# Performance work log

Hardware: AMD Instinct MI355X
Metric: run time of the kernel (lower is better)

Reference implementation:

```python
import jax, jax.numpy as jnp
import numpy as np

H_DIM = 1024
N_HEADS = 16
HEAD_D = H_DIM // N_HEADS  # 64


def setup_inputs() -> dict:
    key = jax.random.key(0)
    ks = jax.random.split(key, 10)
    B, T, C = 2, 2048, H_DIM
    init = 1.0 / np.sqrt(C)  # lecun_normal-scale stand-in
    src = jax.random.normal(ks[0], (B, T, C), dtype=jnp.float32)
    mask = jnp.ones((B, T), dtype=jnp.float32)  # unused when causal
    Wq = jax.random.normal(ks[1], (C, H_DIM), dtype=jnp.float32) * init
    Wk = jax.random.normal(ks[2], (C, H_DIM), dtype=jnp.float32) * init
    Wv = jax.random.normal(ks[3], (C, H_DIM), dtype=jnp.float32) * init
    Wo = jax.random.normal(ks[4], (H_DIM, H_DIM), dtype=jnp.float32) * init
    bq = jnp.zeros((H_DIM,), jnp.float32)
    bk = jnp.zeros((H_DIM,), jnp.float32)
    bv = jnp.zeros((H_DIM,), jnp.float32)
    bo = jnp.zeros((H_DIM,), jnp.float32)
    return {"src": src, "mask": mask, "Wq": Wq, "bq": bq, "Wk": Wk, "bk": bk,
            "Wv": Wv, "bv": bv, "Wo": Wo, "bo": bo}


def reference(src, mask, Wq, bq, Wk, bk, Wv, bv, Wo, bo):
    # MaskedCausalAttention forward, deterministic=True (dropout = identity),
    # use_causal_mask=True.
    B, T, C = src.shape
    N, D = N_HEADS, HEAD_D
    # q,k,v: [B, N, T, D]
    q = (src @ Wq + bq).reshape(B, T, N, D).transpose(0, 2, 1, 3)
    k = (src @ Wk + bk).reshape(B, T, N, D).transpose(0, 2, 1, 3)
    v = (src @ Wv + bv).reshape(B, T, N, D).transpose(0, 2, 1, 3)
    # scores: [B, N, T, T]
    scores = jnp.einsum('bntd,bnsd->bnts', q, k) / jnp.sqrt(jnp.float32(D))
    causal = jnp.tril(jnp.ones((T, T), dtype=bool))[None, None]
    scores = jnp.where(causal, scores, -jnp.inf)
    probs = jax.nn.softmax(scores, axis=-1)
    attn = jnp.einsum('bnts,bnsd->bntd', probs, v)  # [B, N, T, D]
    attn = attn.transpose(0, 2, 1, 3).reshape(B, T, N * D)
    return attn @ Wo + bo
```

## Files before the change

kernel.cpp:

```cpp
#include <hip/hip_runtime.h>
#include <hip/hip_bf16.h>

typedef __hip_bfloat16 bf16;
typedef __attribute__((ext_vector_type(8))) short short8;
typedef __attribute__((ext_vector_type(4))) float f32x4;

#define BATCH 2
#define SEQ   2048
#define HDIM  1024
#define NHEAD 16
#define DHEAD 64
#define MROWS (BATCH*SEQ)

#define QSCALE 0.18033688f
#define EXP2F(x) __builtin_amdgcn_exp2f(x)

static __device__ __forceinline__ short f2bs(float x) {
    __hip_bfloat16 h = (__hip_bfloat16)x;
    return *reinterpret_cast<short*>(&h);
}
static __device__ __forceinline__ unsigned int pk2(float a, float b) {
    __hip_bfloat162 h = __float22bfloat162_rn(make_float2(a, b));
    return *reinterpret_cast<unsigned int*>(&h);
}

static __device__ __forceinline__ void gload16(const void* g, void* l) {
    __builtin_amdgcn_global_load_lds(
        (const __attribute__((address_space(1))) unsigned int*)g,
        (__attribute__((address_space(3))) unsigned int*)l, 16, 0, 0);
}

__global__ __launch_bounds__(256) void prep1(const float* __restrict__ src,
        const float* __restrict__ Wq, const float* __restrict__ Wk,
        const float* __restrict__ Wv,
        short* __restrict__ Sb, short* __restrict__ WqkT,
        short* __restrict__ WvT)
{
    __shared__ float t[64][65];
    const int bx = blockIdx.x, tid = threadIdx.x;
    if (bx < 4096) {
        int i = bx * 256 + tid;
        float4 v = ((const float4*)src)[i];
        ushort4 o;
        o.x = (unsigned short)f2bs(v.x);
        o.y = (unsigned short)f2bs(v.y);
        o.z = (unsigned short)f2bs(v.z);
        o.w = (unsigned short)f2bs(v.w);
        ((ushort4*)Sb)[i] = o;
        return;
    }
    const int tb = bx - 4096;
    const int wsel = tb >> 8;
    const float* W = (wsel == 0) ? Wq : (wsel == 1) ? Wk : Wv;
    short* dst = (wsel < 2) ? WqkT : WvT;
    const int roff = (wsel < 2) ? wsel * 1024 : 0;
    const int t8 = tb & 255;
    const int n0 = (t8 & 15) * 64, k0 = (t8 >> 4) * 64;
#pragma unroll
    for (int i = 0; i < 16; i++) {
        int idx = tid + i * 256, r = idx >> 6, c = idx & 63;
        t[r][c] = W[(size_t)(k0 + r) * HDIM + n0 + c];
    }
    __syncthreads();
#pragma unroll
    for (int i = 0; i < 16; i++) {
        int idx = tid + i * 256, c = idx >> 6, r = idx & 63;
        dst[(size_t)(roff + n0 + c) * HDIM + k0 + r] = f2bs(t[r][c]);
    }
}

__global__ __launch_bounds__(256) void gemm_qk(const short* __restrict__ A,
        const short* __restrict__ Bt,
        const float* __restrict__ bq, const float* __restrict__ bk,
        short* __restrict__ Qout, short* __restrict__ Kout)
{
    __shared__ short As[2][8 * 512];
    __shared__ short Bs[2][8 * 512];
    const int tid = threadIdx.x, lane = tid & 63, w = tid >> 6;
    const int quad = lane >> 4, l15 = lane & 15;
    const int m0 = blockIdx.y * 128, n0 = blockIdx.x * 128;
    const int wr = w >> 1, wc = w & 1;

    const short* gsrc[4];
    short* dst0[4];
    short* dst1[4];
#pragma unroll
    for (int i = 0; i < 4; i++) {
        int u = w * 4 + i;
        if (u < 8) {
            gsrc[i] = A + (size_t)(m0 + u * 16 + l15) * HDIM + quad * 8;
            dst0[i] = &As[0][u * 512];
            dst1[i] = &As[1][u * 512];
        } else {
            int c = u - 8;
            gsrc[i] = Bt + (size_t)(n0 + c * 16 + l15) * HDIM + quad * 8;
            dst0[i] = &Bs[0][c * 512];
            dst1[i] = &Bs[1][c * 512];
        }
    }

    f32x4 acc[4][4];
#pragma unroll
    for (int i = 0; i < 4; i++)
#pragma unroll
        for (int j = 0; j < 4; j++) acc[i][j] = (f32x4){0.f, 0.f, 0.f, 0.f};

#pragma unroll
    for (int i = 0; i < 4; i++) { gload16(gsrc[i], dst0[i]); gsrc[i] += 32; }
    __syncthreads();

    for (int kk = 0; kk < 32; ++kk) {
        const int cur = kk & 1;
        if (kk < 31) {
#pragma unroll
            for (int i = 0; i < 4; i++) {
                gload16(gsrc[i], cur ? dst0[i] : dst1[i]);
                gsrc[i] += 32;
            }
        }
        short8 af[4], bfr[4];
#pragma unroll
        for (int mi = 0; mi < 4; mi++)
            af[mi] = *(const short8*)&As[cur][(wr * 4 + mi) * 512 + lane * 8];
#pragma unroll
        for (int ni = 0; ni < 4; ni++)
            bfr[ni] = *(const short8*)&Bs[cur][(wc * 4 + ni) * 512 + lane * 8];
#pragma unroll
        for (int mi = 0; mi < 4; mi++)
#pragma unroll
            for (int ni = 0; ni < 4; ni++)
                acc[mi][ni] = __builtin_amdgcn_mfma_f32_16x16x32_bf16(
                                  af[mi], bfr[ni], acc[mi][ni], 0, 0, 0);
        __syncthreads();
    }

    const int region = n0 >> 10;
    const float* bias = region ? bk : bq;
    const float oscale = region ? 1.0f : QSCALE;
    short* C = region ? Kout : Qout;

#pragma unroll
    for (int mi = 0; mi < 4; mi++) {
        int mB = m0 + (wr * 4 + mi) * 16 + quad * 4;
#pragma unroll
        for (int ni = 0; ni < 4; ni++) {
            int nl = (n0 + (wc * 4 + ni) * 16 + l15) & 1023;
            float bb = bias[nl];
#pragma unroll
            for (int r = 0; r < 4; r++)
                C[(size_t)(mB + r) * HDIM + nl] =
                    f2bs((acc[mi][ni][r] + bb) * oscale);
        }
    }
}

__global__ __launch_bounds__(256) void gemm_v(const short* __restrict__ A,
        const short* __restrict__ Bt, const float* __restrict__ bv,
        short* __restrict__ Vtout)
{
    __shared__ short As[2][4 * 512];
    __shared__ short Bs[2][8 * 512];
    const int tid = threadIdx.x, lane = tid & 63, w = tid >> 6;
    const int quad = lane >> 4, l15 = lane & 15;
    const int m0 = blockIdx.y * 64, n0 = blockIdx.x * 128;
    const int wr = w >> 1, wc = w & 1;

    const short* gsrc[3];
    short* dst0[3];
    short* dst1[3];
#pragma unroll
    for (int i = 0; i < 3; i++) {
        int u = w * 3 + i;
        if (u < 4) {
            gsrc[i] = A + (size_t)(m0 + u * 16 + l15) * HDIM + quad * 8;
            dst0[i] = &As[0][u * 512];
            dst1[i] = &As[1][u * 512];
        } else {
            int c = u - 4;
            gsrc[i] = Bt + (size_t)(n0 + c * 16 + l15) * HDIM + quad * 8;
            dst0[i] = &Bs[0][c * 512];
            dst1[i] = &Bs[1][c * 512];
        }
    }

    f32x4 acc[2][4];
#pragma unroll
    for (int i = 0; i < 2; i++)
#pragma unroll
        for (int j = 0; j < 4; j++) acc[i][j] = (f32x4){0.f, 0.f, 0.f, 0.f};

#pragma unroll
    for (int i = 0; i < 3; i++) { gload16(gsrc[i], dst0[i]); gsrc[i] += 32; }
    __syncthreads();

    for (int kk = 0; kk < 32; ++kk) {
        const int cur = kk & 1;
        if (kk < 31) {
#pragma unroll
            for (int i = 0; i < 3; i++) {
                gload16(gsrc[i], cur ? dst0[i] : dst1[i]);
                gsrc[i] += 32;
            }
        }
        short8 af[2], bfr[4];
#pragma unroll
        for (int mi = 0; mi < 2; mi++)
            af[mi] = *(const short8*)&As[cur][(wr * 2 + mi) * 512 + lane * 8];
#pragma unroll
        for (int ni = 0; ni < 4; ni++)
            bfr[ni] = *(const short8*)&Bs[cur][(wc * 4 + ni) * 512 + lane * 8];
#pragma unroll
        for (int mi = 0; mi < 2; mi++)
#pragma unroll
            for (int ni = 0; ni < 4; ni++)
                acc[mi][ni] = __builtin_amdgcn_mfma_f32_16x16x32_bf16(
                                  af[mi], bfr[ni], acc[mi][ni], 0, 0, 0);
        __syncthreads();
    }

#pragma unroll
    for (int mi = 0; mi < 2; mi++) {
        int mB = m0 + (wr * 2 + mi) * 16 + quad * 4;
        int bb = mB >> 11, t = mB & 2047;
#pragma unroll
        for (int ni = 0; ni < 4; ni++) {
            int n = n0 + (wc * 4 + ni) * 16 + l15;
            int h = n >> 6, d = n & 63;
            float bvv = bv[n];
            size_t base = ((size_t)((bb * NHEAD + h) * DHEAD + d)) * SEQ + t;
            ushort4 pk;
            pk.x = (unsigned short)f2bs(acc[mi][ni][0] + bvv);
            pk.y = (unsigned short)f2bs(acc[mi][ni][1] + bvv);
            pk.z = (unsigned short)f2bs(acc[mi][ni][2] + bvv);
            pk.w = (unsigned short)f2bs(acc[mi][ni][3] + bvv);
            *(ushort4*)(Vtout + base) = pk;
        }
    }
}

__global__ __launch_bounds__(256) void gemm_o(const short* __restrict__ A,
        const short* __restrict__ Bt, const float* __restrict__ bo,
        float* __restrict__ Out)
{
    __shared__ short As[2][4 * 512];
    __shared__ short Bs[2][8 * 512];
    const int tid = threadIdx.x, lane = tid & 63, w = tid >> 6;
    const int quad = lane >> 4, l15 = lane & 15;
    const int m0 = blockIdx.y * 64, n0 = blockIdx.x * 128;
    const int wr = w >> 1, wc = w & 1;

    const short* gsrc[3];
    short* dst0[3];
    short* dst1[3];
#pragma unroll
    for (int i = 0; i < 3; i++) {
        int u = w * 3 + i;
        if (u < 4) {
            gsrc[i] = A + (size_t)(m0 + u * 16 + l15) * HDIM + quad * 8;
            dst0[i] = &As[0][u * 512];
            dst1[i] = &As[1][u * 512];
        } else {
            int c = u - 4;
            gsrc[i] = Bt + (size_t)(n0 + c * 16 + l15) * HDIM + quad * 8;
            dst0[i] = &Bs[0][c * 512];
            dst1[i] = &Bs[1][c * 512];
        }
    }

    f32x4 acc[2][4];
#pragma unroll
    for (int i = 0; i < 2; i++)
#pragma unroll
        for (int j = 0; j < 4; j++) acc[i][j] = (f32x4){0.f, 0.f, 0.f, 0.f};

#pragma unroll
    for (int i = 0; i < 3; i++) { gload16(gsrc[i], dst0[i]); gsrc[i] += 32; }
    __syncthreads();

    for (int kk = 0; kk < 32; ++kk) {
        const int cur = kk & 1;
        if (kk < 31) {
#pragma unroll
            for (int i = 0; i < 3; i++) {
                gload16(gsrc[i], cur ? dst0[i] : dst1[i]);
                gsrc[i] += 32;
            }
        }
        short8 af[2], bfr[4];
#pragma unroll
        for (int mi = 0; mi < 2; mi++)
            af[mi] = *(const short8*)&As[cur][(wr * 2 + mi) * 512 + lane * 8];
#pragma unroll
        for (int ni = 0; ni < 4; ni++)
            bfr[ni] = *(const short8*)&Bs[cur][(wc * 4 + ni) * 512 + lane * 8];
#pragma unroll
        for (int mi = 0; mi < 2; mi++)
#pragma unroll
            for (int ni = 0; ni < 4; ni++)
                acc[mi][ni] = __builtin_amdgcn_mfma_f32_16x16x32_bf16(
                                  af[mi], bfr[ni], acc[mi][ni], 0, 0, 0);
        __syncthreads();
    }

#pragma unroll
    for (int mi = 0; mi < 2; mi++) {
        int mB = m0 + (wr * 2 + mi) * 16 + quad * 4;
#pragma unroll
        for (int ni = 0; ni < 4; ni++) {
            int n = n0 + (wc * 4 + ni) * 16 + l15;
            float bb = bo[n];
#pragma unroll
            for (int r = 0; r < 4; r++)
                Out[(size_t)(mB + r) * HDIM + n] = acc[mi][ni][r] + bb;
        }
    }
}

__global__ __launch_bounds__(256) void attn_mfma(const short* __restrict__ Qb,
        const short* __restrict__ Kb, const short* __restrict__ Vt,
        short* __restrict__ Ab,
        const float* __restrict__ Wo, short* __restrict__ WoT)
{
    __shared__ short SMEM[21248];
    short* Ks = SMEM;
    short* Vs = SMEM + 8192;
    short* Ps = SMEM + 16384;
    const int tid = threadIdx.x, lane = tid & 63, w = tid >> 6;
    const int quad = lane >> 4, l15 = lane & 15;

    if (blockIdx.x == 16) {
        float* t = (float*)SMEM;
        const int bsel = blockIdx.z * 16 + blockIdx.y;
#pragma unroll
        for (int j = 0; j < 8; j++) {
            int t8 = bsel * 8 + j;
            int n0 = (t8 & 15) * 64, k0 = (t8 >> 4) * 64;
            __syncthreads();
#pragma unroll
            for (int i = 0; i < 16; i++) {
                int idx = tid + i * 256, r = idx >> 6, c = idx & 63;
                t[r * 65 + c] = Wo[(size_t)(k0 + r) * HDIM + n0 + c];
            }
            __syncthreads();
#pragma unroll
            for (int i = 0; i < 16; i++) {
                int idx = tid + i * 256, c = idx >> 6, r = idx & 63;
                WoT[(size_t)(n0 + c) * HDIM + k0 + r] = f2bs(t[r * 65 + c]);
            }
        }
        return;
    }

    const int L = blockIdx.x + 16 * (blockIdx.y + 16 * blockIdx.z);
    const int slot = L >> 3;
    const int pair = (L & 7) * 4 + (slot >> 4);
    const int strip0 = slot & 15;
    const int b = pair >> 4, head = pair & 15;

    const short* Kbh = Kb + (size_t)b * SEQ * HDIM + head * DHEAD;
    const short* Vth = Vt + (size_t)(b * NHEAD + head) * DHEAD * SEQ;
    short* Pw = &Ps[w * 1152];

    auto stage = [&](int s0, int bf) {
#pragma unroll
        for (int i = 0; i < 4; i++) {
            int u = w * 4 + i;
            if (u < 8) {
                int t = u >> 1, h = u & 1;
                const short* g = Kbh + (size_t)(s0 + t * 16 + l15) * HDIM
                                 + h * 32 + quad * 8;
                gload16(g, &Ks[bf * 4096 + u * 512]);
            } else {
                int c = u - 8, dt = c >> 1, kh = c & 1;
                const short* g = Vth + (size_t)(dt * 16 + l15) * SEQ
                                 + s0 + kh * 32 + quad * 8;
                gload16(g, &Vs[bf * 4096 + c * 512]);
            }
        }
    };

    const int strips[2] = { strip0, 31 - strip0 };

    for (int si = 0; si < 2; ++si) {
        const int strip = strips[si];
        const int qbase = strip * 64;
        const int qr = qbase + w * 16 + l15;

        const short* qptr = Qb + (size_t)(b * SEQ + qr) * HDIM + head * DHEAD + quad * 8;
        short8 bq0 = *(const short8*)qptr;
        short8 bq1 = *(const short8*)(qptr + 32);

        f32x4 o[4];
#pragma unroll
        for (int dt = 0; dt < 4; dt++) o[dt] = (f32x4){0.f, 0.f, 0.f, 0.f};
        float psum = 0.f;

        stage(0, 0);
        __syncthreads();

        for (int it = 0; it <= strip; ++it) {
            const int s0 = it * 64;
            const int cur = it & 1;
            if (it < strip) stage(s0 + 64, cur ^ 1);

            f32x4 sv[4];
#pragma unroll
            for (int t = 0; t < 4; t++) {
                sv[t] = (f32x4){0.f, 0.f, 0.f, 0.f};
                short8 k0 = *(const short8*)&Ks[cur * 4096 + (t * 2) * 512 + lane * 8];
                short8 k1 = *(const short8*)&Ks[cur * 4096 + (t * 2 + 1) * 512 + lane * 8];
                sv[t] = __builtin_amdgcn_mfma_f32_16x16x32_bf16(k0, bq0, sv[t], 0, 0, 0);
                sv[t] = __builtin_amdgcn_mfma_f32_16x16x32_bf16(k1, bq1, sv[t], 0, 0, 0);
            }

            float p[16];
            if (it == strip) {
#pragma unroll
                for (int t = 0; t < 4; t++)
#pragma unroll
                    for (int r = 0; r < 4; r++) {
                        int key = s0 + t * 16 + quad * 4 + r;
                        p[t * 4 + r] = (key <= qr) ? EXP2F(sv[t][r]) : 0.f;
                    }
            } else {
#pragma unroll
                for (int t = 0; t < 4; t++)
#pragma unroll
                    for (int r = 0; r < 4; r++)
                        p[t * 4 + r] = EXP2F(sv[t][r]);
            }
#pragma unroll
            for (int i = 0; i < 16; i++) psum += p[i];

#pragma unroll
            for (int t = 0; t < 4; t++) {
                uint2 u2;
                u2.x = pk2(p[t * 4],     p[t * 4 + 1]);
                u2.y = pk2(p[t * 4 + 2], p[t * 4 + 3]);
                *(uint2*)&Pw[l15 * 72 + t * 16 + quad * 4] = u2;
            }
            short8 bp0 = *(const short8*)&Pw[l15 * 72 + quad * 8];
            short8 bp1 = *(const short8*)&Pw[l15 * 72 + 32 + quad * 8];

#pragma unroll
            for (int dt = 0; dt < 4; dt++) {
                short8 av0 = *(const short8*)&Vs[cur * 4096 + (dt * 2) * 512 + lane * 8];
                short8 av1 = *(const short8*)&Vs[cur * 4096 + (dt * 2 + 1) * 512 + lane * 8];
                o[dt] = __builtin_amdgcn_mfma_f32_16x16x32_bf16(av0, bp0, o[dt], 0, 0, 0);
                o[dt] = __builtin_amdgcn_mfma_f32_16x16x32_bf16(av1, bp1, o[dt], 0, 0, 0);
            }
            __syncthreads();
        }

        float lrow = psum + __shfl_xor(psum, 16);
        lrow += __shfl_xor(lrow, 32);
        const float inv = 1.f / lrow;

        const size_t obase = (size_t)(b * SEQ + qr) * HDIM + head * DHEAD;
#pragma unroll
        for (int dt = 0; dt < 4; dt++) {
            uint2 u2;
            u2.x = pk2(o[dt][0] * inv, o[dt][1] * inv);
            u2.y = pk2(o[dt][2] * inv, o[dt][3] * inv);
            *(uint2*)&Ab[obase + dt * 16 + quad * 4] = u2;
        }
    }
}

extern "C" void kernel_launch(void* const* d_in, const int* in_sizes, int n_in,
                              void* d_out, int out_size, void* d_ws, size_t ws_size,
                              hipStream_t stream)
{
    const float* src = (const float*)d_in[0];
    const float* Wq = (const float*)d_in[2];
    const float* bq = (const float*)d_in[3];
    const float* Wk = (const float*)d_in[4];
    const float* bk = (const float*)d_in[5];
    const float* Wv = (const float*)d_in[6];
    const float* bv = (const float*)d_in[7];
    const float* Wo = (const float*)d_in[8];
    const float* bo = (const float*)d_in[9];
    float* out = (float*)d_out;

    short* Sb   = (short*)d_ws;
    short* Qb   = Sb + (size_t)MROWS * HDIM;
    short* Kb   = Qb + (size_t)MROWS * HDIM;
    short* Vt   = Kb + (size_t)MROWS * HDIM;
    short* slot = Vt + (size_t)MROWS * HDIM;
    short* WqkT = Vt;
    short* Ab   = Qb;

    dim3 blk(256);

    prep1<<<dim3(4096 + 768), blk, 0, stream>>>(src, Wq, Wk, Wv, Sb, WqkT, slot);

    gemm_qk<<<dim3(16, 32), blk, 0, stream>>>(Sb, WqkT, bq, bk, Qb, Kb);

    gemm_v<<<dim3(8, 64), blk, 0, stream>>>(Sb, slot, bv, Vt);

    attn_mfma<<<dim3(17, NHEAD, BATCH), blk, 0, stream>>>(Qb, Kb, Vt, Ab, Wo, slot);

    gemm_o<<<dim3(8, 64), blk, 0, stream>>>(Ab, slot, bo, out);
}
```

Before: 232.1 us.

## Split attention into one-strip blocks, drop K/V double buffering, shrink QK GEMM tiles

The attention kernel no longer pairs a short and a long query strip per block. It now launches one block per strip, 1024 blocks plus 32 for the Wo transpose, ordered longest strip first so the load stays balanced across the GPU. Shared memory drops from 21248 to 12800 shorts by removing the double-buffered K/V staging, which should allow more resident blocks but exposes load latency on every iteration. The Q/K projection GEMM is also retiled from 128x128 to 64x128 blocks, doubling its grid.

```diff
diff --git a/kernel.cpp b/kernel.cpp
--- a/kernel.cpp
+++ b/kernel.cpp
@@ -74,90 +74,6 @@
         const float* __restrict__ bq, const float* __restrict__ bk,
         short* __restrict__ Qout, short* __restrict__ Kout)
 {
-    __shared__ short As[2][8 * 512];
-    __shared__ short Bs[2][8 * 512];
-    const int tid = threadIdx.x, lane = tid & 63, w = tid >> 6;
-    const int quad = lane >> 4, l15 = lane & 15;
-    const int m0 = blockIdx.y * 128, n0 = blockIdx.x * 128;
-    const int wr = w >> 1, wc = w & 1;
-
-    const short* gsrc[4];
-    short* dst0[4];
-    short* dst1[4];
-#pragma unroll
-    for (int i = 0; i < 4; i++) {
-        int u = w * 4 + i;
-        if (u < 8) {
-            gsrc[i] = A + (size_t)(m0 + u * 16 + l15) * HDIM + quad * 8;
-            dst0[i] = &As[0][u * 512];
-            dst1[i] = &As[1][u * 512];
-        } else {
-            int c = u - 8;
-            gsrc[i] = Bt + (size_t)(n0 + c * 16 + l15) * HDIM + quad * 8;
-            dst0[i] = &Bs[0][c * 512];
-            dst1[i] = &Bs[1][c * 512];
-        }
-    }
-
-    f32x4 acc[4][4];
-#pragma unroll
-    for (int i = 0; i < 4; i++)
-#pragma unroll
-        for (int j = 0; j < 4; j++) acc[i][j] = (f32x4){0.f, 0.f, 0.f, 0.f};
-
-#pragma unroll
-    for (int i = 0; i < 4; i++) { gload16(gsrc[i], dst0[i]); gsrc[i] += 32; }
-    __syncthreads();
-
-    for (int kk = 0; kk < 32; ++kk) {
-        const int cur = kk & 1;
-        if (kk < 31) {
-#pragma unroll
-            for (int i = 0; i < 4; i++) {
-                gload16(gsrc[i], cur ? dst0[i] : dst1[i]);
-                gsrc[i] += 32;
-            }
-        }
-        short8 af[4], bfr[4];
-#pragma unroll
-        for (int mi = 0; mi < 4; mi++)
-            af[mi] = *(const short8*)&As[cur][(wr * 4 + mi) * 512 + lane * 8];
-#pragma unroll
-        for (int ni = 0; ni < 4; ni++)
-            bfr[ni] = *(const short8*)&Bs[cur][(wc * 4 + ni) * 512 + lane * 8];
-#pragma unroll
-        for (int mi = 0; mi < 4; mi++)
-#pragma unroll
-            for (int ni = 0; ni < 4; ni++)
-                acc[mi][ni] = __builtin_amdgcn_mfma_f32_16x16x32_bf16(
-                                  af[mi], bfr[ni], acc[mi][ni], 0, 0, 0);
-        __syncthreads();
-    }
-
-    const int region = n0 >> 10;
-    const float* bias = region ? bk : bq;
-    const float oscale = region ? 1.0f : QSCALE;
-    short* C = region ? Kout : Qout;
-
-#pragma unroll
-    for (int mi = 0; mi < 4; mi++) {
-        int mB = m0 + (wr * 4 + mi) * 16 + quad * 4;
-#pragma unroll
-        for (int ni = 0; ni < 4; ni++) {
-            int nl = (n0 + (wc * 4 + ni) * 16 + l15) & 1023;
-            float bb = bias[nl];
-#pragma unroll
-            for (int r = 0; r < 4; r++)
-                C[(size_t)(mB + r) * HDIM + nl] =
-                    f2bs((acc[mi][ni][r] + bb) * oscale);
-        }
-    }
-}
-
-__global__ __launch_bounds__(256) void gemm_v(const short* __restrict__ A,
-        const short* __restrict__ Bt, const float* __restrict__ bv,
-        short* __restrict__ Vtout)
-{
     __shared__ short As[2][4 * 512];
     __shared__ short Bs[2][8 * 512];
     const int tid = threadIdx.x, lane = tid & 63, w = tid >> 6;
@@ -218,6 +134,90 @@
         __syncthreads();
     }
 
+    const int region = n0 >> 10;
+    const float* bias = region ? bk : bq;
+    const float oscale = region ? 1.0f : QSCALE;
+    short* C = region ? Kout : Qout;
+
+#pragma unroll
+    for (int mi = 0; mi < 2; mi++) {
+        int mB = m0 + (wr * 2 + mi) * 16 + quad * 4;
+#pragma unroll
+        for (int ni = 0; ni < 4; ni++) {
+            int nl = (n0 + (wc * 4 + ni) * 16 + l15) & 1023;
+            float bb = bias[nl];
+#pragma unroll
+            for (int r = 0; r < 4; r++)
+                C[(size_t)(mB + r) * HDIM + nl] =
+                    f2bs((acc[mi][ni][r] + bb) * oscale);
+        }
+    }
+}
+
+__global__ __launch_bounds__(256) void gemm_v(const short* __restrict__ A,
+        const short* __restrict__ Bt, const float* __restrict__ bv,
+        short* __restrict__ Vtout)
+{
+    __shared__ short As[2][4 * 512];
+    __shared__ short Bs[2][8 * 512];
+    const int tid = threadIdx.x, lane = tid & 63, w = tid >> 6;
+    const int quad = lane >> 4, l15 = lane & 15;
+    const int m0 = blockIdx.y * 64, n0 = blockIdx.x * 128;
+    const int wr = w >> 1, wc = w & 1;
+
+    const short* gsrc[3];
+    short* dst0[3];
+    short* dst1[3];
+#pragma unroll
+    for (int i = 0; i < 3; i++) {
+        int u = w * 3 + i;
+        if (u < 4) {
+            gsrc[i] = A + (size_t)(m0 + u * 16 + l15) * HDIM + quad * 8;
+            dst0[i] = &As[0][u * 512];
+            dst1[i] = &As[1][u * 512];
+        } else {
+            int c = u - 4;
+            gsrc[i] = Bt + (size_t)(n0 + c * 16 + l15) * HDIM + quad * 8;
+            dst0[i] = &Bs[0][c * 512];
+            dst1[i] = &Bs[1][c * 512];
+        }
+    }
+
+    f32x4 acc[2][4];
+#pragma unroll
+    for (int i = 0; i < 2; i++)
+#pragma unroll
+        for (int j = 0; j < 4; j++) acc[i][j] = (f32x4){0.f, 0.f, 0.f, 0.f};
+
+#pragma unroll
+    for (int i = 0; i < 3; i++) { gload16(gsrc[i], dst0[i]); gsrc[i] += 32; }
+    __syncthreads();
+
+    for (int kk = 0; kk < 32; ++kk) {
+        const int cur = kk & 1;
+        if (kk < 31) {
+#pragma unroll
+            for (int i = 0; i < 3; i++) {
+                gload16(gsrc[i], cur ? dst0[i] : dst1[i]);
+                gsrc[i] += 32;
+            }
+        }
+        short8 af[2], bfr[4];
+#pragma unroll
+        for (int mi = 0; mi < 2; mi++)
+            af[mi] = *(const short8*)&As[cur][(wr * 2 + mi) * 512 + lane * 8];
+#pragma unroll
+        for (int ni = 0; ni < 4; ni++)
+            bfr[ni] = *(const short8*)&Bs[cur][(wc * 4 + ni) * 512 + lane * 8];
+#pragma unroll
+        for (int mi = 0; mi < 2; mi++)
+#pragma unroll
+            for (int ni = 0; ni < 4; ni++)
+                acc[mi][ni] = __builtin_amdgcn_mfma_f32_16x16x32_bf16(
+                                  af[mi], bfr[ni], acc[mi][ni], 0, 0, 0);
+        __syncthreads();
+    }
+
 #pragma unroll
     for (int mi = 0; mi < 2; mi++) {
         int mB = m0 + (wr * 2 + mi) * 16 + quad * 4;
@@ -321,16 +321,17 @@
         short* __restrict__ Ab,
         const float* __restrict__ Wo, short* __restrict__ WoT)
 {
-    __shared__ short SMEM[21248];
+    __shared__ short SMEM[12800];
     short* Ks = SMEM;
-    short* Vs = SMEM + 8192;
-    short* Ps = SMEM + 16384;
+    short* Vs = SMEM + 4096;
+    short* Ps = SMEM + 8192;
     const int tid = threadIdx.x, lane = tid & 63, w = tid >> 6;
     const int quad = lane >> 4, l15 = lane & 15;
-
-    if (blockIdx.x == 16) {
+    const int L = blockIdx.x;
+
+    if (L >= 1024) {
         float* t = (float*)SMEM;
-        const int bsel = blockIdx.z * 16 + blockIdx.y;
+        const int bsel = L - 1024;
 #pragma unroll
         for (int j = 0; j < 8; j++) {
             int t8 = bsel * 8 + j;
@@ -351,119 +352,103 @@
         return;
     }
 
-    const int L = blockIdx.x + 16 * (blockIdx.y + 16 * blockIdx.z);
-    const int slot = L >> 3;
-    const int pair = (L & 7) * 4 + (slot >> 4);
-    const int strip0 = slot & 15;
+    const int pair = (L & 7) + 8 * ((L >> 3) & 3);
+    const int strip = 31 - (L >> 5);
     const int b = pair >> 4, head = pair & 15;
 
     const short* Kbh = Kb + (size_t)b * SEQ * HDIM + head * DHEAD;
     const short* Vth = Vt + (size_t)(b * NHEAD + head) * DHEAD * SEQ;
     short* Pw = &Ps[w * 1152];
 
-    auto stage = [&](int s0, int bf) {
+    const int qbase = strip * 64;
+    const int qr = qbase + w * 16 + l15;
+
+    const short* qptr = Qb + (size_t)(b * SEQ + qr) * HDIM + head * DHEAD + quad * 8;
+    short8 bq0 = *(const short8*)qptr;
+    short8 bq1 = *(const short8*)(qptr + 32);
+
+    f32x4 o[4];
+#pragma unroll
+    for (int dt = 0; dt < 4; dt++) o[dt] = (f32x4){0.f, 0.f, 0.f, 0.f};
+    float psum = 0.f;
+
+    for (int it = 0; it <= strip; ++it) {
+        const int s0 = it * 64;
 #pragma unroll
         for (int i = 0; i < 4; i++) {
             int u = w * 4 + i;
             if (u < 8) {
                 int t = u >> 1, h = u & 1;
-                const short* g = Kbh + (size_t)(s0 + t * 16 + l15) * HDIM
-                                 + h * 32 + quad * 8;
-                gload16(g, &Ks[bf * 4096 + u * 512]);
+                gload16(Kbh + (size_t)(s0 + t * 16 + l15) * HDIM + h * 32 + quad * 8,
+                        &Ks[u * 512]);
             } else {
                 int c = u - 8, dt = c >> 1, kh = c & 1;
-                const short* g = Vth + (size_t)(dt * 16 + l15) * SEQ
-                                 + s0 + kh * 32 + quad * 8;
-                gload16(g, &Vs[bf * 4096 + c * 512]);
-            }
-        }
-    };
-
-    const int strips[2] = { strip0, 31 - strip0 };
-
-    for (int si = 0; si < 2; ++si) {
-        const int strip = strips[si];
-        const int qbase = strip * 64;
-        const int qr = qbase + w * 16 + l15;
-
-        const short* qptr = Qb + (size_t)(b * SEQ + qr) * HDIM + head * DHEAD + quad * 8;
-        short8 bq0 = *(const short8*)qptr;
-        short8 bq1 = *(const short8*)(qptr + 32);
-
-        f32x4 o[4];
-#pragma unroll
-        for (int dt = 0; dt < 4; dt++) o[dt] = (f32x4){0.f, 0.f, 0.f, 0.f};
-        float psum = 0.f;
-
-        stage(0, 0);
+                gload16(Vth + (size_t)(dt * 16 + l15) * SEQ + s0 + kh * 32 + quad * 8,
+                        &Vs[c * 512]);
+            }
+        }
         __syncthreads();
 
-        for (int it = 0; it <= strip; ++it) {
-            const int s0 = it * 64;
-            const int cur = it & 1;
-            if (it < strip) stage(s0 + 64, cur ^ 1);
-
-            f32x4 sv[4];
-#pragma unroll
-            for (int t = 0; t < 4; t++) {
-                sv[t] = (f32x4){0.f, 0.f, 0.f, 0.f};
-                short8 k0 = *(const short8*)&Ks[cur * 4096 + (t * 2) * 512 + lane * 8];
-                short8 k1 = *(const short8*)&Ks[cur * 4096 + (t * 2 + 1) * 512 + lane * 8];
-                sv[t] = __builtin_amdgcn_mfma_f32_16x16x32_bf16(k0, bq0, sv[t], 0, 0, 0);
-                sv[t] = __builtin_amdgcn_mfma_f32_16x16x32_bf16(k1, bq1, sv[t], 0, 0, 0);
-            }
-
-            float p[16];
-            if (it == strip) {
-#pragma unroll
-                for (int t = 0; t < 4; t++)
-#pragma unroll
-                    for (int r = 0; r < 4; r++) {
-                        int key = s0 + t * 16 + quad * 4 + r;
-                        p[t * 4 + r] = (key <= qr) ? EXP2F(sv[t][r]) : 0.f;
-                    }
-            } else {
-#pragma unroll
-                for (int t = 0; t < 4; t++)
-#pragma unroll
-                    for (int r = 0; r < 4; r++)
-                        p[t * 4 + r] = EXP2F(sv[t][r]);
-            }
-#pragma unroll
-            for (int i = 0; i < 16; i++) psum += p[i];
-
-#pragma unroll
-            for (int t = 0; t < 4; t++) {
-                uint2 u2;
-                u2.x = pk2(p[t * 4],     p[t * 4 + 1]);
-                u2.y = pk2(p[t * 4 + 2], p[t * 4 + 3]);
-                *(uint2*)&Pw[l15 * 72 + t * 16 + quad * 4] = u2;
-            }
-            short8 bp0 = *(const short8*)&Pw[l15 * 72 + quad * 8];
-            short8 bp1 = *(const short8*)&Pw[l15 * 72 + 32 + quad * 8];
-
-#pragma unroll
-            for (int dt = 0; dt < 4; dt++) {
-                short8 av0 = *(const short8*)&Vs[cur * 4096 + (dt * 2) * 512 + lane * 8];
-                short8 av1 = *(const short8*)&Vs[cur * 4096 + (dt * 2 + 1) * 512 + lane * 8];
-                o[dt] = __builtin_amdgcn_mfma_f32_16x16x32_bf16(av0, bp0, o[dt], 0, 0, 0);
-                o[dt] = __builtin_amdgcn_mfma_f32_16x16x32_bf16(av1, bp1, o[dt], 0, 0, 0);
-            }
-            __syncthreads();
-        }
-
-        float lrow = psum + __shfl_xor(psum, 16);
-        lrow += __shfl_xor(lrow, 32);
-        const float inv = 1.f / lrow;
-
-        const size_t obase = (size_t)(b * SEQ + qr) * HDIM + head * DHEAD;
+        f32x4 sv[4];
+#pragma unroll
+        for (int t = 0; t < 4; t++) {
+            sv[t] = (f32x4){0.f, 0.f, 0.f, 0.f};
+            short8 k0 = *(const short8*)&Ks[(t * 2) * 512 + lane * 8];
+            short8 k1 = *(const short8*)&Ks[(t * 2 + 1) * 512 + lane * 8];
+            sv[t] = __builtin_amdgcn_mfma_f32_16x16x32_bf16(k0, bq0, sv[t], 0, 0, 0);
+            sv[t] = __builtin_amdgcn_mfma_f32_16x16x32_bf16(k1, bq1, sv[t], 0, 0, 0);
+        }
+
+        float p[16];
+        if (it == strip) {
+#pragma unroll
+            for (int t = 0; t < 4; t++)
+#pragma unroll
+                for (int r = 0; r < 4; r++) {
+                    int key = s0 + t * 16 + quad * 4 + r;
+                    p[t * 4 + r] = (key <= qr) ? EXP2F(sv[t][r]) : 0.f;
+                }
+        } else {
+#pragma unroll
+            for (int t = 0; t < 4; t++)
+#pragma unroll
+                for (int r = 0; r < 4; r++)
+                    p[t * 4 + r] = EXP2F(sv[t][r]);
+        }
+#pragma unroll
+        for (int i = 0; i < 16; i++) psum += p[i];
+
+#pragma unroll
+        for (int t = 0; t < 4; t++) {
+            uint2 u2;
+            u2.x = pk2(p[t * 4],     p[t * 4 + 1]);
+            u2.y = pk2(p[t * 4 + 2], p[t * 4 + 3]);
+            *(uint2*)&Pw[l15 * 72 + t * 16 + quad * 4] = u2;
+        }
+        short8 bp0 = *(const short8*)&Pw[l15 * 72 + quad * 8];
+        short8 bp1 = *(const short8*)&Pw[l15 * 72 + 32 + quad * 8];
+
 #pragma unroll
         for (int dt = 0; dt < 4; dt++) {
-            uint2 u2;
-            u2.x = pk2(o[dt][0] * inv, o[dt][1] * inv);
-            u2.y = pk2(o[dt][2] * inv, o[dt][3] * inv);
-            *(uint2*)&Ab[obase + dt * 16 + quad * 4] = u2;
-        }
+            short8 av0 = *(const short8*)&Vs[(dt * 2) * 512 + lane * 8];
+            short8 av1 = *(const short8*)&Vs[(dt * 2 + 1) * 512 + lane * 8];
+            o[dt] = __builtin_amdgcn_mfma_f32_16x16x32_bf16(av0, bp0, o[dt], 0, 0, 0);
+            o[dt] = __builtin_amdgcn_mfma_f32_16x16x32_bf16(av1, bp1, o[dt], 0, 0, 0);
+        }
+        __syncthreads();
+    }
+
+    float lrow = psum + __shfl_xor(psum, 16);
+    lrow += __shfl_xor(lrow, 32);
+    const float inv = 1.f / lrow;
+
+    const size_t obase = (size_t)(b * SEQ + qr) * HDIM + head * DHEAD;
+#pragma unroll
+    for (int dt = 0; dt < 4; dt++) {
+        uint2 u2;
+        u2.x = pk2(o[dt][0] * inv, o[dt][1] * inv);
+        u2.y = pk2(o[dt][2] * inv, o[dt][3] * inv);
+        *(uint2*)&Ab[obase + dt * 16 + quad * 4] = u2;
     }
 }
 
@@ -494,11 +479,11 @@
 
     prep1<<<dim3(4096 + 768), blk, 0, stream>>>(src, Wq, Wk, Wv, Sb, WqkT, slot);
 
-    gemm_qk<<<dim3(16, 32), blk, 0, stream>>>(Sb, WqkT, bq, bk, Qb, Kb);
+    gemm_qk<<<dim3(16, 64), blk, 0, stream>>>(Sb, WqkT, bq, bk, Qb, Kb);
 
     gemm_v<<<dim3(8, 64), blk, 0, stream>>>(Sb, slot, bv, Vt);
 
-    attn_mfma<<<dim3(17, NHEAD, BATCH), blk, 0, stream>>>(Qb, Kb, Vt, Ab, Wo, slot);
+    attn_mfma<<<dim3(1024 + 32), blk, 0, stream>>>(Qb, Kb, Vt, Ab, Wo, slot);
 
     gemm_o<<<dim3(8, 64), blk, 0, stream>>>(Ab, slot, bo, out);
 }
```

After: 240.3 us. 1.04x slower.
